# Optimization experiments

Measured on AMD Instinct MI355X. Metric: run time of the kernel, lower is better.

The kernel has to match this reference:

```python
import jax, jax.numpy as jnp
import numpy as np
from functools import partial

DELTA_B = 30.0
DELTA_H = 30.0
NB = 12  # 360/30
NH = 12
E, H, A, MLP, T = 16, 32, 32, 128, 20


def setup_inputs() -> dict:
    key = jax.random.key(0)
    ks = jax.random.split(key, 32)
    B, N = 512, 32
    inp = {}
    inp['x'] = jax.random.normal(ks[0], (B, N, T, 2), jnp.float32)
    inp['dmat'] = jax.random.uniform(ks[1], (B, N, T, N), jnp.float32) * 10.0
    inp['bmat'] = jax.random.uniform(ks[2], (B, N, T, N), jnp.float32) * 360.0
    inp['hmat'] = jax.random.uniform(ks[3], (B, N, T, N), jnp.float32) * 360.0
    inp['mask'] = jnp.ones((B, N, T), jnp.float32)
    g = lambda k, sh, s=0.1: jax.random.normal(k, sh, jnp.float32) * s
    inp['emb_w'] = g(ks[4], (2, E)); inp['emb_b'] = jnp.zeros((E,), jnp.float32)
    inp['w_ih'] = g(ks[5], (E, 4 * H)); inp['w_hh'] = g(ks[6], (H, 4 * H))
    inp['b_ih'] = jnp.zeros((4 * H,), jnp.float32); inp['b_hh'] = jnp.zeros((4 * H,), jnp.float32)
    inp['enc2att_w'] = g(ks[7], (H, A)); inp['enc2att_b'] = jnp.zeros((A,), jnp.float32)
    inp['domain_tab'] = jnp.full((NB, NH), 5.0, jnp.float32)  # domain_parameter init
    inp['spemb_w'] = g(ks[8], (2 * A, A)); inp['spemb_b'] = jnp.zeros((A,), jnp.float32)
    inp['att2enc_w'] = g(ks[9], (A, H)); inp['att2enc_b'] = jnp.zeros((H,), jnp.float32)
    inp['cls_w1'] = g(ks[10], (T * H, MLP)); inp['cls_b1'] = jnp.zeros((MLP,), jnp.float32)
    inp['cls_w2'] = g(ks[11], (MLP, MLP)); inp['cls_b2'] = jnp.zeros((MLP,), jnp.float32)
    inp['cls_w3'] = g(ks[12], (MLP, 1)); inp['cls_b3'] = jnp.zeros((1,), jnp.float32)
    return inp


def _forward(x, dmat, bmat, hmat, mask, emb_w, emb_b, w_ih, w_hh, b_ih, b_hh,
             enc2att_w, enc2att_b, domain_tab, spemb_w, spemb_b,
             att2enc_w, att2enc_b, cls_w1, cls_b1, cls_w2, cls_b2, cls_w3, cls_b3):
    B, N = x.shape[0], x.shape[1]
    xe = x @ emb_w + emb_b                      # [B,N,T,E]
    # time-major sequences for scan
    seq = (jnp.moveaxis(xe, 2, 0), jnp.moveaxis(dmat, 2, 0), jnp.moveaxis(bmat, 2, 0),
           jnp.moveaxis(hmat, 2, 0), jnp.moveaxis(mask, 2, 0))
    h0 = jnp.zeros((B, N, H), xe.dtype)
    c0 = jnp.zeros((B, N, H), xe.dtype)

    def step(carry, inp):
        h, c = carry
        x_t, d_t, b_t, hd_t, m_t = inp
        gates = x_t @ w_ih + h @ w_hh + (b_ih + b_hh)   # [B,N,4H]
        i, f, g, o = jnp.split(gates, 4, axis=-1)
        c_new = jax.nn.sigmoid(f) * c + jax.nn.sigmoid(i) * jnp.tanh(g)
        h_lstm = jax.nn.sigmoid(o) * jnp.tanh(c_new)
        ha = h_lstm @ enc2att_w + enc2att_b              # enc2att -> [B,N,A]
        # spatial attention: domain value from bearing/heading bins vs distance
        ib = jnp.clip(jnp.floor(b_t / DELTA_B), 0, NB - 1).astype(jnp.int32)
        ih = jnp.clip(jnp.floor(hd_t / DELTA_H), 0, NH - 1).astype(jnp.int32)
        w = jax.nn.relu(domain_tab[ib, ih] - d_t)        # [B,N,N]
        w = w * m_t[:, :, None] * m_t[:, None, :]
        w = w / (w.sum(-1, keepdims=True) + 1e-8)
        att = jnp.einsum('bij,bjd->bid', w, ha)          # neighbor-weighted hidden
        emb = jnp.tanh(jnp.concatenate([ha, att], -1) @ spemb_w + spemb_b)
        h_new = emb @ att2enc_w + att2enc_b              # back to hidden_size
        return (h_new, c_new), h_new

    (_, _), hs = jax.lax.scan(step, (h0, c0), seq)       # hs: [T,B,N,H]
    enc = jnp.moveaxis(hs, 0, 2).reshape(B, N, T * H)
    z = jax.nn.leaky_relu(enc @ cls_w1 + cls_b1, 0.2)
    z = jax.nn.leaky_relu(z @ cls_w2 + cls_b2, 0.2)
    return jax.nn.sigmoid(z @ cls_w3 + cls_b3)           # [B,N,1]


def reference(x, dmat, bmat, hmat, mask, emb_w, emb_b, w_ih, w_hh, b_ih, b_hh,
              enc2att_w, enc2att_b, domain_tab, spemb_w, spemb_b,
              att2enc_w, att2enc_b, cls_w1, cls_b1, cls_w2, cls_b2, cls_w3, cls_b3):
    return _forward(x, dmat, bmat, hmat, mask, emb_w, emb_b, w_ih, w_hh, b_ih, b_hh,
                    enc2att_w, enc2att_b, domain_tab, spemb_w, spemb_b,
                    att2enc_w, att2enc_b, cls_w1, cls_b1, cls_w2, cls_b2, cls_w3, cls_b3)
```

## Files before the change

kernel.cpp:

```cpp
#include <hip/hip_runtime.h>
#include <hip/hip_bf16.h>

#define TD_B 512

typedef __bf16 bf16x8 __attribute__((ext_vector_type(8)));
typedef __bf16 bf16x4 __attribute__((ext_vector_type(4)));
typedef float  f32x4  __attribute__((ext_vector_type(4)));

#define MFMA(a, b, c) __builtin_amdgcn_mfma_f32_16x16x32_bf16((a), (b), (c), 0, 0, 0)

__device__ __forceinline__ float sigf(float x)  { return 1.0f / (1.0f + __expf(-x)); }
__device__ __forceinline__ float tanhf_(float x){ return 2.0f / (1.0f + __expf(-2.0f * x)) - 1.0f; }

extern "C" __global__ void __launch_bounds__(256, 2)
traj_disc_kernel(const float* __restrict__ x, const float* __restrict__ dmat,
                 const float* __restrict__ bmat, const float* __restrict__ hmat,
                 const float* __restrict__ mask,
                 const float* __restrict__ emb_w, const float* __restrict__ emb_b,
                 const float* __restrict__ w_ih, const float* __restrict__ w_hh,
                 const float* __restrict__ b_ih, const float* __restrict__ b_hh,
                 const float* __restrict__ e2a_w, const float* __restrict__ e2a_b,
                 const float* __restrict__ dom,
                 const float* __restrict__ sp_w, const float* __restrict__ sp_b,
                 const float* __restrict__ a2e_w, const float* __restrict__ a2e_b,
                 const float* __restrict__ w1, const float* __restrict__ b1,
                 const float* __restrict__ w2, const float* __restrict__ b2,
                 const float* __restrict__ w3, const float* __restrict__ b3,
                 float* __restrict__ out)
{
    const int b    = blockIdx.x;
    const int tid  = threadIdx.x;
    const int lane = tid & 63;
    const int w    = tid >> 6;
    const int l15  = lane & 15;
    const int lg   = lane >> 4;

    __shared__ __bf16 sAin[32][72];
    __shared__ __bf16 sHl [32][40];
    __shared__ __bf16 sWN [32][40];
    __shared__ __bf16 sHaT[32][40];
    __shared__ __bf16 sEmb[32][40];
    __shared__ __bf16 sPA [32][72];
    __shared__ float  sMaskT[20][36];
    __shared__ float  sDom[144];
    __shared__ __bf16 z1bf[32][136];
    __shared__ __bf16 z2bf[32][136];

    for (int idx = tid; idx < 32 * 72; idx += 256)
        (&sAin[0][0])[idx] = (idx % 72 == 48) ? (__bf16)1.0f : (__bf16)0.0f;
    for (int idx = tid; idx < 640; idx += 256) {
        int tt = idx >> 5, n = idx & 31;
        sMaskT[tt][n] = mask[(b * 32 + n) * 20 + tt];
    }
    if (tid < 144) sDom[tid] = dom[tid];

    const int i0 = tid >> 3, p0 = tid & 7;
    const float ewa0 = emb_w[2 * p0],      ewa1 = emb_w[2 * p0 + 1];
    const float ewb0 = emb_w[16 + 2 * p0], ewb1 = emb_w[16 + 2 * p0 + 1];
    const float eb0  = emb_b[2 * p0],      eb1  = emb_b[2 * p0 + 1];

    bf16x8 Ag[2][2];
    #pragma unroll
    for (int mtl = 0; mtl < 2; ++mtl) {
        int c  = (2 * w + mtl) * 16 + l15;
        int cg = (c & 3) * 32 + (c >> 2);
        #pragma unroll
        for (int kt = 0; kt < 2; ++kt)
            #pragma unroll
            for (int j = 0; j < 8; ++j) {
                int k = kt * 32 + lg * 8 + j;
                float v;
                if (k < 16)       v = w_ih[k * 128 + cg];
                else if (k < 48)  v = w_hh[(k - 16) * 128 + cg];
                else if (k == 48) v = b_ih[cg] + b_hh[cg];
                else              v = 0.0f;
                Ag[mtl][kt][j] = (__bf16)v;
            }
    }
    const int mtw = w >> 1, ntw = w & 1;
    const int cw  = ntw * 16 + l15;
    bf16x8 Be2a, Ba2e, Bsp[2];
    #pragma unroll
    for (int j = 0; j < 8; ++j) {
        Be2a[j] = (__bf16)e2a_w[(lg * 8 + j) * 32 + cw];
        Ba2e[j] = (__bf16)a2e_w[(lg * 8 + j) * 32 + cw];
    }
    #pragma unroll
    for (int kt = 0; kt < 2; ++kt)
        #pragma unroll
        for (int j = 0; j < 8; ++j)
            Bsp[kt][j] = (__bf16)sp_w[(kt * 32 + lg * 8 + j) * 32 + cw];
    const float bEw = e2a_b[cw], bSw = sp_b[cw], bAw = a2e_b[cw];

    float cst[2][2] = {{0.f, 0.f}, {0.f, 0.f}};
    f32x4 accZ[2][2] = {};
    bf16x8 Bw1cur[2];

    float4 pdv, pbv, phv; float px0, px1;
    {
        int base = ((b * 32 + i0) * 20 + 0) * 32 + 4 * p0;
        pdv = *(const float4*)(dmat + base);
        pbv = *(const float4*)(bmat + base);
        phv = *(const float4*)(hmat + base);
        int xb = ((b * 32 + i0) * 20 + 0) * 2;
        px0 = x[xb]; px1 = x[xb + 1];
    }
    __syncthreads();

    #pragma unroll 1
    for (int t = 0; t < 20; ++t) {
        {
            float4 dv = pdv, bv = pbv, hv = phv;
            float xx0 = px0, xx1 = px1;
            if (t < 19) {
                int base = ((b * 32 + i0) * 20 + (t + 1)) * 32 + 4 * p0;
                pdv = *(const float4*)(dmat + base);
                pbv = *(const float4*)(bmat + base);
                phv = *(const float4*)(hmat + base);
                int xb = ((b * 32 + i0) * 20 + (t + 1)) * 2;
                px0 = x[xb]; px1 = x[xb + 1];
            }
            float4 mj = *(const float4*)&sMaskT[t][4 * p0];
            float  mi = sMaskT[t][i0];
            float wq[4];
            #pragma unroll
            for (int q = 0; q < 4; ++q) {
                float bq = (&bv.x)[q], hq = (&hv.x)[q];
                int ib = (int)floorf(bq * (1.0f / 30.0f)); ib = ib < 0 ? 0 : (ib > 11 ? 11 : ib);
                int ih = (int)floorf(hq * (1.0f / 30.0f)); ih = ih < 0 ? 0 : (ih > 11 ? 11 : ih);
                float v = sDom[ib * 12 + ih] - (&dv.x)[q];
                v = v > 0.f ? v : 0.f;
                wq[q] = v * (&mj.x)[q];
            }
            float s = wq[0] + wq[1] + wq[2] + wq[3];
            s += __shfl_xor(s, 1); s += __shfl_xor(s, 2); s += __shfl_xor(s, 4);
            float inv = mi / (mi * s + 1e-8f);
            bf16x4 wn4;
            #pragma unroll
            for (int q = 0; q < 4; ++q) wn4[q] = (__bf16)(wq[q] * inv);
            *(bf16x4*)&sWN[i0][4 * p0] = wn4;
            sAin[i0][2 * p0]     = (__bf16)(xx0 * ewa0 + xx1 * ewb0 + eb0);
            sAin[i0][2 * p0 + 1] = (__bf16)(xx0 * ewa1 + xx1 * ewb1 + eb1);
        }
        __syncthreads();

        {
            bf16x8 bxh[2][2];
            #pragma unroll
            for (int nt = 0; nt < 2; ++nt)
                #pragma unroll
                for (int kt = 0; kt < 2; ++kt)
                    bxh[nt][kt] = *(const bf16x8*)&sAin[nt * 16 + l15][kt * 32 + lg * 8];
            if (t >= 1) {
                bf16x8 az[2];
                #pragma unroll
                for (int mt = 0; mt < 2; ++mt)
                    az[mt] = *(const bf16x8*)&sAin[mt * 16 + l15][16 + lg * 8];
                #pragma unroll
                for (int mt = 0; mt < 2; ++mt)
                    #pragma unroll
                    for (int ntp = 0; ntp < 2; ++ntp)
                        accZ[mt][ntp] = MFMA(az[mt], Bw1cur[ntp], accZ[mt][ntp]);
            }
            #pragma unroll
            for (int mtl = 0; mtl < 2; ++mtl)
                #pragma unroll
                for (int nt = 0; nt < 2; ++nt) {
                    f32x4 cc = {0.f, 0.f, 0.f, 0.f};
                    cc = MFMA(Ag[mtl][0], bxh[nt][0], cc);
                    cc = MFMA(Ag[mtl][1], bxh[nt][1], cc);
                    float cn = sigf(cc[1]) * cst[mtl][nt] + sigf(cc[0]) * tanhf_(cc[2]);
                    cst[mtl][nt] = cn;
                    sHl[nt * 16 + l15][4 * (2 * w + mtl) + lg] = (__bf16)(sigf(cc[3]) * tanhf_(cn));
                }
            #pragma unroll
            for (int ntp = 0; ntp < 2; ++ntp) {
                int c = (2 * w + ntp) * 16 + l15;
                #pragma unroll
                for (int j = 0; j < 8; ++j)
                    Bw1cur[ntp][j] = (__bf16)w1[(t * 32 + lg * 8 + j) * 128 + c];
            }
        }
        __syncthreads();

        {
            bf16x8 a = *(const bf16x8*)&sHl[mtw * 16 + l15][lg * 8];
            f32x4 cc = {0.f, 0.f, 0.f, 0.f};
            cc = MFMA(a, Be2a, cc);
            bf16x4 tv;
            #pragma unroll
            for (int q = 0; q < 4; ++q) {
                float v = cc[q] + bEw;
                tv[q] = (__bf16)v;
                sPA[mtw * 16 + 4 * lg + q][cw] = (__bf16)v;
            }
            *(bf16x4*)&sHaT[cw][mtw * 16 + 4 * lg] = tv;
        }
        __syncthreads();

        {
            bf16x8 aW = *(const bf16x8*)&sWN [mtw * 16 + l15][lg * 8];
            bf16x8 bT = *(const bf16x8*)&sHaT[cw][lg * 8];
            f32x4 cc = {0.f, 0.f, 0.f, 0.f};
            cc = MFMA(aW, bT, cc);
            #pragma unroll
            for (int q = 0; q < 4; ++q)
                sPA[mtw * 16 + 4 * lg + q][32 + cw] = (__bf16)cc[q];
        }
        __syncthreads();

        {
            bf16x8 a0 = *(const bf16x8*)&sPA[mtw * 16 + l15][lg * 8];
            bf16x8 a1 = *(const bf16x8*)&sPA[mtw * 16 + l15][32 + lg * 8];
            f32x4 cc = {0.f, 0.f, 0.f, 0.f};
            cc = MFMA(a0, Bsp[0], cc);
            cc = MFMA(a1, Bsp[1], cc);
            #pragma unroll
            for (int q = 0; q < 4; ++q)
                sEmb[mtw * 16 + 4 * lg + q][cw] = (__bf16)tanhf_(cc[q] + bSw);
        }
        __syncthreads();

        {
            bf16x8 a = *(const bf16x8*)&sEmb[mtw * 16 + l15][lg * 8];
            f32x4 cc = {0.f, 0.f, 0.f, 0.f};
            cc = MFMA(a, Ba2e, cc);
            #pragma unroll
            for (int q = 0; q < 4; ++q)
                sAin[mtw * 16 + 4 * lg + q][16 + cw] = (__bf16)(cc[q] + bAw);
        }
        __syncthreads();
    }

    {
        bf16x8 az[2];
        #pragma unroll
        for (int mt = 0; mt < 2; ++mt)
            az[mt] = *(const bf16x8*)&sAin[mt * 16 + l15][16 + lg * 8];
        #pragma unroll
        for (int mt = 0; mt < 2; ++mt)
            #pragma unroll
            for (int ntp = 0; ntp < 2; ++ntp)
                accZ[mt][ntp] = MFMA(az[mt], Bw1cur[ntp], accZ[mt][ntp]);
    }
    #pragma unroll
    for (int mt = 0; mt < 2; ++mt)
        #pragma unroll
        for (int ntp = 0; ntp < 2; ++ntp) {
            int c = (2 * w + ntp) * 16 + l15;
            float bias = b1[c];
            #pragma unroll
            for (int q = 0; q < 4; ++q) {
                float v = accZ[mt][ntp][q] + bias;
                v = v > 0.f ? v : 0.2f * v;
                z1bf[mt * 16 + 4 * lg + q][c] = (__bf16)v;
            }
        }
    __syncthreads();

    {
        f32x4 c2[2][2] = {};
        #pragma unroll
        for (int kt = 0; kt < 4; ++kt) {
            bf16x8 a[2];
            #pragma unroll
            for (int mt = 0; mt < 2; ++mt)
                a[mt] = *(const bf16x8*)&z1bf[mt * 16 + l15][kt * 32 + lg * 8];
            bf16x8 bb[2];
            #pragma unroll
            for (int ntp = 0; ntp < 2; ++ntp) {
                int c = (2 * w + ntp) * 16 + l15;
                #pragma unroll
                for (int j = 0; j < 8; ++j)
                    bb[ntp][j] = (__bf16)w2[(kt * 32 + lg * 8 + j) * 128 + c];
            }
            #pragma unroll
            for (int mt = 0; mt < 2; ++mt)
                #pragma unroll
                for (int ntp = 0; ntp < 2; ++ntp)
                    c2[mt][ntp] = MFMA(a[mt], bb[ntp], c2[mt][ntp]);
        }
        #pragma unroll
        for (int mt = 0; mt < 2; ++mt)
            #pragma unroll
            for (int ntp = 0; ntp < 2; ++ntp) {
                int c = (2 * w + ntp) * 16 + l15;
                float bias = b2[c];
                #pragma unroll
                for (int q = 0; q < 4; ++q) {
                    float v = c2[mt][ntp][q] + bias;
                    v = v > 0.f ? v : 0.2f * v;
                    z2bf[mt * 16 + 4 * lg + q][c] = (__bf16)v;
                }
            }
    }
    __syncthreads();

    {
        int n = tid >> 3, kg = tid & 7;
        bf16x8 v0 = *(const bf16x8*)&z2bf[n][kg * 16];
        bf16x8 v1 = *(const bf16x8*)&z2bf[n][kg * 16 + 8];
        float s = 0.f;
        #pragma unroll
        for (int j = 0; j < 8; ++j)
            s += (float)v0[j] * w3[kg * 16 + j] + (float)v1[j] * w3[kg * 16 + 8 + j];
        s += __shfl_xor(s, 1); s += __shfl_xor(s, 2); s += __shfl_xor(s, 4);
        if (kg == 0) out[b * 32 + n] = sigf(s + b3[0]);
    }
}

extern "C" void kernel_launch(void* const* d_in, const int* in_sizes, int n_in,
                              void* d_out, int out_size, void* d_ws, size_t ws_size,
                              hipStream_t stream) {
    (void)in_sizes; (void)n_in; (void)d_ws; (void)ws_size; (void)out_size;
    const float* x     = (const float*)d_in[0];
    const float* dmat  = (const float*)d_in[1];
    const float* bmat  = (const float*)d_in[2];
    const float* hmat  = (const float*)d_in[3];
    const float* mask  = (const float*)d_in[4];
    const float* emb_w = (const float*)d_in[5];
    const float* emb_b = (const float*)d_in[6];
    const float* w_ih  = (const float*)d_in[7];
    const float* w_hh  = (const float*)d_in[8];
    const float* b_ih  = (const float*)d_in[9];
    const float* b_hh  = (const float*)d_in[10];
    const float* e2a_w = (const float*)d_in[11];
    const float* e2a_b = (const float*)d_in[12];
    const float* dom   = (const float*)d_in[13];
    const float* sp_w  = (const float*)d_in[14];
    const float* sp_b  = (const float*)d_in[15];
    const float* a2e_w = (const float*)d_in[16];
    const float* a2e_b = (const float*)d_in[17];
    const float* w1    = (const float*)d_in[18];
    const float* b1    = (const float*)d_in[19];
    const float* w2    = (const float*)d_in[20];
    const float* b2    = (const float*)d_in[21];
    const float* w3    = (const float*)d_in[22];
    const float* b3    = (const float*)d_in[23];
    float* out = (float*)d_out;

    traj_disc_kernel<<<dim3(TD_B), dim3(256), 0, stream>>>(
        x, dmat, bmat, hmat, mask, emb_w, emb_b, w_ih, w_hh, b_ih, b_hh,
        e2a_w, e2a_b, dom, sp_w, sp_b, a2e_w, a2e_b,
        w1, b1, w2, b2, w3, b3, out);
}
```

Measured before the change: 72.71 us.

## Process two batch items per 512-thread block and merge attention stages

Each block now handles two batch elements with 8 waves instead of one with 4, so the LSTM gate weights (Ag) are held once per wave and applied to 64 rows. The per-step pipeline merges the e2a, attention and spemb/a2e stages so they share fewer barriers, dropping from six to three __syncthreads per timestep. The w1 prefetch is moved to the start of the step so its latency overlaps more work. The grid halves to 256 blocks, which on a many-CU GPU may leave CUs idle and raises per-block LDS and register pressure.

```diff
diff --git a/kernel.cpp b/kernel.cpp
--- a/kernel.cpp
+++ b/kernel.cpp
@@ -1,7 +1,5 @@
 #include <hip/hip_runtime.h>
 #include <hip/hip_bf16.h>
-
-#define TD_B 512
 
 typedef __bf16 bf16x8 __attribute__((ext_vector_type(8)));
 typedef __bf16 bf16x4 __attribute__((ext_vector_type(4)));
@@ -12,7 +10,7 @@
 __device__ __forceinline__ float sigf(float x)  { return 1.0f / (1.0f + __expf(-x)); }
 __device__ __forceinline__ float tanhf_(float x){ return 2.0f / (1.0f + __expf(-2.0f * x)) - 1.0f; }
 
-extern "C" __global__ void __launch_bounds__(256, 2)
+extern "C" __global__ void __launch_bounds__(512, 2)
 traj_disc_kernel(const float* __restrict__ x, const float* __restrict__ dmat,
                  const float* __restrict__ bmat, const float* __restrict__ hmat,
                  const float* __restrict__ mask,
@@ -28,41 +26,42 @@
                  const float* __restrict__ w3, const float* __restrict__ b3,
                  float* __restrict__ out)
 {
-    const int b    = blockIdx.x;
+    const int b0   = blockIdx.x * 2;
     const int tid  = threadIdx.x;
     const int lane = tid & 63;
     const int w    = tid >> 6;
     const int l15  = lane & 15;
     const int lg   = lane >> 4;
 
-    __shared__ __bf16 sAin[32][72];
-    __shared__ __bf16 sHl [32][40];
-    __shared__ __bf16 sWN [32][40];
-    __shared__ __bf16 sHaT[32][40];
-    __shared__ __bf16 sEmb[32][40];
-    __shared__ __bf16 sPA [32][72];
-    __shared__ float  sMaskT[20][36];
+    __shared__ __bf16 sAin[64][72];
+    __shared__ __bf16 sHl [64][40];
+    __shared__ __bf16 sWN [64][40];
+    __shared__ __bf16 sHaT[64][40];
+    __shared__ __bf16 sEmb[64][40];
+    __shared__ __bf16 sPA [64][72];
+    __shared__ float  sMaskT[20][2][36];
     __shared__ float  sDom[144];
-    __shared__ __bf16 z1bf[32][136];
-    __shared__ __bf16 z2bf[32][136];
-
-    for (int idx = tid; idx < 32 * 72; idx += 256)
+    __shared__ __bf16 z1bf[64][136];
+    __shared__ __bf16 z2bf[64][136];
+
+    for (int idx = tid; idx < 64 * 72; idx += 512)
         (&sAin[0][0])[idx] = (idx % 72 == 48) ? (__bf16)1.0f : (__bf16)0.0f;
-    for (int idx = tid; idx < 640; idx += 256) {
-        int tt = idx >> 5, n = idx & 31;
-        sMaskT[tt][n] = mask[(b * 32 + n) * 20 + tt];
+    for (int idx = tid; idx < 1280; idx += 512) {
+        int tt = idx >> 6, r = idx & 63;
+        sMaskT[tt][r >> 5][r & 31] = mask[((b0 + (r >> 5)) * 32 + (r & 31)) * 20 + tt];
     }
     if (tid < 144) sDom[tid] = dom[tid];
 
     const int i0 = tid >> 3, p0 = tid & 7;
+    const int wbA = i0 >> 5, iA = i0 & 31;
+    const int bbA = b0 + wbA;
     const float ewa0 = emb_w[2 * p0],      ewa1 = emb_w[2 * p0 + 1];
     const float ewb0 = emb_w[16 + 2 * p0], ewb1 = emb_w[16 + 2 * p0 + 1];
     const float eb0  = emb_b[2 * p0],      eb1  = emb_b[2 * p0 + 1];
 
-    bf16x8 Ag[2][2];
-    #pragma unroll
-    for (int mtl = 0; mtl < 2; ++mtl) {
-        int c  = (2 * w + mtl) * 16 + l15;
+    bf16x8 Ag[2];
+    {
+        int c  = 16 * w + l15;
         int cg = (c & 3) * 32 + (c >> 2);
         #pragma unroll
         for (int kt = 0; kt < 2; ++kt)
@@ -74,12 +73,12 @@
                 else if (k < 48)  v = w_hh[(k - 16) * 128 + cg];
                 else if (k == 48) v = b_ih[cg] + b_hh[cg];
                 else              v = 0.0f;
-                Ag[mtl][kt][j] = (__bf16)v;
-            }
-    }
-    const int mtw = w >> 1, ntw = w & 1;
-    const int cw  = ntw * 16 + l15;
-    bf16x8 Be2a, Ba2e, Bsp[2];
+                Ag[kt][j] = (__bf16)v;
+            }
+    }
+    const int wb = w >> 2, mtw = (w >> 1) & 1, ntw = w & 1;
+    const int cw = ntw * 16 + l15;
+    bf16x8 Be2a, Ba2e, Bsp[2][2];
     #pragma unroll
     for (int j = 0; j < 8; ++j) {
         Be2a[j] = (__bf16)e2a_w[(lg * 8 + j) * 32 + cw];
@@ -88,21 +87,25 @@
     #pragma unroll
     for (int kt = 0; kt < 2; ++kt)
         #pragma unroll
-        for (int j = 0; j < 8; ++j)
-            Bsp[kt][j] = (__bf16)sp_w[(kt * 32 + lg * 8 + j) * 32 + cw];
-    const float bEw = e2a_b[cw], bSw = sp_b[cw], bAw = a2e_b[cw];
-
-    float cst[2][2] = {{0.f, 0.f}, {0.f, 0.f}};
-    f32x4 accZ[2][2] = {};
-    bf16x8 Bw1cur[2];
+        for (int nt2 = 0; nt2 < 2; ++nt2)
+            #pragma unroll
+            for (int j = 0; j < 8; ++j)
+                Bsp[kt][nt2][j] = (__bf16)sp_w[(kt * 32 + lg * 8 + j) * 32 + nt2 * 16 + l15];
+    const float bEw = e2a_b[cw], bAw = a2e_b[cw];
+    const float bS2[2] = { sp_b[l15], sp_b[16 + l15] };
+
+    float cst[4] = {0.f, 0.f, 0.f, 0.f};
+    f32x4 accZ[4] = {};
+    bf16x8 Bw1cur, Bw1nxt;
+    const int c1 = 16 * w + l15;
 
     float4 pdv, pbv, phv; float px0, px1;
     {
-        int base = ((b * 32 + i0) * 20 + 0) * 32 + 4 * p0;
+        int base = ((bbA * 32 + iA) * 20 + 0) * 32 + 4 * p0;
         pdv = *(const float4*)(dmat + base);
         pbv = *(const float4*)(bmat + base);
         phv = *(const float4*)(hmat + base);
-        int xb = ((b * 32 + i0) * 20 + 0) * 2;
+        int xb = ((bbA * 32 + iA) * 20 + 0) * 2;
         px0 = x[xb]; px1 = x[xb + 1];
     }
     __syncthreads();
@@ -110,18 +113,21 @@
     #pragma unroll 1
     for (int t = 0; t < 20; ++t) {
         {
+            #pragma unroll
+            for (int j = 0; j < 8; ++j)
+                Bw1nxt[j] = (__bf16)w1[(t * 32 + lg * 8 + j) * 128 + c1];
             float4 dv = pdv, bv = pbv, hv = phv;
             float xx0 = px0, xx1 = px1;
             if (t < 19) {
-                int base = ((b * 32 + i0) * 20 + (t + 1)) * 32 + 4 * p0;
+                int base = ((bbA * 32 + iA) * 20 + (t + 1)) * 32 + 4 * p0;
                 pdv = *(const float4*)(dmat + base);
                 pbv = *(const float4*)(bmat + base);
                 phv = *(const float4*)(hmat + base);
-                int xb = ((b * 32 + i0) * 20 + (t + 1)) * 2;
+                int xb = ((bbA * 32 + iA) * 20 + (t + 1)) * 2;
                 px0 = x[xb]; px1 = x[xb + 1];
             }
-            float4 mj = *(const float4*)&sMaskT[t][4 * p0];
-            float  mi = sMaskT[t][i0];
+            float4 mj = *(const float4*)&sMaskT[t][wbA][4 * p0];
+            float  mi = sMaskT[t][wbA][iA];
             float wq[4];
             #pragma unroll
             for (int q = 0; q < 4; ++q) {
@@ -145,167 +151,132 @@
         __syncthreads();
 
         {
-            bf16x8 bxh[2][2];
-            #pragma unroll
-            for (int nt = 0; nt < 2; ++nt)
+            bf16x8 az[4], bxh[4][2];
+            #pragma unroll
+            for (int rt = 0; rt < 4; ++rt) {
+                az[rt]     = *(const bf16x8*)&sAin[rt * 16 + l15][16 + lg * 8];
+                bxh[rt][0] = *(const bf16x8*)&sAin[rt * 16 + l15][lg * 8];
+                bxh[rt][1] = *(const bf16x8*)&sAin[rt * 16 + l15][32 + lg * 8];
+            }
+            if (t >= 1) {
                 #pragma unroll
-                for (int kt = 0; kt < 2; ++kt)
-                    bxh[nt][kt] = *(const bf16x8*)&sAin[nt * 16 + l15][kt * 32 + lg * 8];
-            if (t >= 1) {
-                bf16x8 az[2];
+                for (int rt = 0; rt < 4; ++rt)
+                    accZ[rt] = MFMA(az[rt], Bw1cur, accZ[rt]);
+            }
+            Bw1cur = Bw1nxt;
+            #pragma unroll
+            for (int rt = 0; rt < 4; ++rt) {
+                f32x4 cc = {0.f, 0.f, 0.f, 0.f};
+                cc = MFMA(Ag[0], bxh[rt][0], cc);
+                cc = MFMA(Ag[1], bxh[rt][1], cc);
+                float cn = sigf(cc[1]) * cst[rt] + sigf(cc[0]) * tanhf_(cc[2]);
+                cst[rt] = cn;
+                sHl[rt * 16 + l15][4 * w + lg] = (__bf16)(sigf(cc[3]) * tanhf_(cn));
+            }
+        }
+        __syncthreads();
+
+        {
+            #pragma unroll
+            for (int mt = 0; mt < 2; ++mt) {
+                bf16x8 a = *(const bf16x8*)&sHl[wb * 32 + mt * 16 + l15][lg * 8];
+                f32x4 cc = {0.f, 0.f, 0.f, 0.f};
+                cc = MFMA(a, Be2a, cc);
+                bf16x4 tv;
                 #pragma unroll
-                for (int mt = 0; mt < 2; ++mt)
-                    az[mt] = *(const bf16x8*)&sAin[mt * 16 + l15][16 + lg * 8];
-                #pragma unroll
-                for (int mt = 0; mt < 2; ++mt)
-                    #pragma unroll
-                    for (int ntp = 0; ntp < 2; ++ntp)
-                        accZ[mt][ntp] = MFMA(az[mt], Bw1cur[ntp], accZ[mt][ntp]);
-            }
-            #pragma unroll
-            for (int mtl = 0; mtl < 2; ++mtl)
-                #pragma unroll
-                for (int nt = 0; nt < 2; ++nt) {
-                    f32x4 cc = {0.f, 0.f, 0.f, 0.f};
-                    cc = MFMA(Ag[mtl][0], bxh[nt][0], cc);
-                    cc = MFMA(Ag[mtl][1], bxh[nt][1], cc);
-                    float cn = sigf(cc[1]) * cst[mtl][nt] + sigf(cc[0]) * tanhf_(cc[2]);
-                    cst[mtl][nt] = cn;
-                    sHl[nt * 16 + l15][4 * (2 * w + mtl) + lg] = (__bf16)(sigf(cc[3]) * tanhf_(cn));
+                for (int q = 0; q < 4; ++q) {
+                    float v = cc[q] + bEw;
+                    tv[q] = (__bf16)v;
+                    sPA[wb * 32 + mt * 16 + 4 * lg + q][cw] = (__bf16)v;
                 }
-            #pragma unroll
-            for (int ntp = 0; ntp < 2; ++ntp) {
-                int c = (2 * w + ntp) * 16 + l15;
-                #pragma unroll
-                for (int j = 0; j < 8; ++j)
-                    Bw1cur[ntp][j] = (__bf16)w1[(t * 32 + lg * 8 + j) * 128 + c];
-            }
-        }
-        __syncthreads();
-
-        {
-            bf16x8 a = *(const bf16x8*)&sHl[mtw * 16 + l15][lg * 8];
-            f32x4 cc = {0.f, 0.f, 0.f, 0.f};
-            cc = MFMA(a, Be2a, cc);
-            bf16x4 tv;
-            #pragma unroll
-            for (int q = 0; q < 4; ++q) {
-                float v = cc[q] + bEw;
-                tv[q] = (__bf16)v;
-                sPA[mtw * 16 + 4 * lg + q][cw] = (__bf16)v;
-            }
-            *(bf16x4*)&sHaT[cw][mtw * 16 + 4 * lg] = tv;
-        }
-        __syncthreads();
-
-        {
-            bf16x8 aW = *(const bf16x8*)&sWN [mtw * 16 + l15][lg * 8];
-            bf16x8 bT = *(const bf16x8*)&sHaT[cw][lg * 8];
+                *(bf16x4*)&sHaT[wb * 32 + cw][mt * 16 + 4 * lg] = tv;
+            }
+            bf16x8 aW = *(const bf16x8*)&sWN [wb * 32 + mtw * 16 + l15][lg * 8];
+            bf16x8 bT = *(const bf16x8*)&sHaT[wb * 32 + ntw * 16 + l15][lg * 8];
             f32x4 cc = {0.f, 0.f, 0.f, 0.f};
             cc = MFMA(aW, bT, cc);
             #pragma unroll
             for (int q = 0; q < 4; ++q)
-                sPA[mtw * 16 + 4 * lg + q][32 + cw] = (__bf16)cc[q];
+                sPA[wb * 32 + mtw * 16 + 4 * lg + q][32 + cw] = (__bf16)cc[q];
         }
         __syncthreads();
 
         {
-            bf16x8 a0 = *(const bf16x8*)&sPA[mtw * 16 + l15][lg * 8];
-            bf16x8 a1 = *(const bf16x8*)&sPA[mtw * 16 + l15][32 + lg * 8];
-            f32x4 cc = {0.f, 0.f, 0.f, 0.f};
-            cc = MFMA(a0, Bsp[0], cc);
-            cc = MFMA(a1, Bsp[1], cc);
+            bf16x8 a0 = *(const bf16x8*)&sPA[wb * 32 + mtw * 16 + l15][lg * 8];
+            bf16x8 a1 = *(const bf16x8*)&sPA[wb * 32 + mtw * 16 + l15][32 + lg * 8];
+            #pragma unroll
+            for (int nt2 = 0; nt2 < 2; ++nt2) {
+                f32x4 cc = {0.f, 0.f, 0.f, 0.f};
+                cc = MFMA(a0, Bsp[0][nt2], cc);
+                cc = MFMA(a1, Bsp[1][nt2], cc);
+                #pragma unroll
+                for (int q = 0; q < 4; ++q)
+                    sEmb[wb * 32 + mtw * 16 + 4 * lg + q][nt2 * 16 + l15] = (__bf16)tanhf_(cc[q] + bS2[nt2]);
+            }
+            bf16x8 ae = *(const bf16x8*)&sEmb[wb * 32 + mtw * 16 + l15][lg * 8];
+            f32x4 cf = {0.f, 0.f, 0.f, 0.f};
+            cf = MFMA(ae, Ba2e, cf);
             #pragma unroll
             for (int q = 0; q < 4; ++q)
-                sEmb[mtw * 16 + 4 * lg + q][cw] = (__bf16)tanhf_(cc[q] + bSw);
-        }
-        __syncthreads();
-
-        {
-            bf16x8 a = *(const bf16x8*)&sEmb[mtw * 16 + l15][lg * 8];
-            f32x4 cc = {0.f, 0.f, 0.f, 0.f};
-            cc = MFMA(a, Ba2e, cc);
-            #pragma unroll
-            for (int q = 0; q < 4; ++q)
-                sAin[mtw * 16 + 4 * lg + q][16 + cw] = (__bf16)(cc[q] + bAw);
-        }
-        __syncthreads();
-    }
-
-    {
-        bf16x8 az[2];
-        #pragma unroll
-        for (int mt = 0; mt < 2; ++mt)
-            az[mt] = *(const bf16x8*)&sAin[mt * 16 + l15][16 + lg * 8];
-        #pragma unroll
-        for (int mt = 0; mt < 2; ++mt)
-            #pragma unroll
-            for (int ntp = 0; ntp < 2; ++ntp)
-                accZ[mt][ntp] = MFMA(az[mt], Bw1cur[ntp], accZ[mt][ntp]);
-    }
-    #pragma unroll
-    for (int mt = 0; mt < 2; ++mt)
-        #pragma unroll
-        for (int ntp = 0; ntp < 2; ++ntp) {
-            int c = (2 * w + ntp) * 16 + l15;
-            float bias = b1[c];
+                sAin[wb * 32 + mtw * 16 + 4 * lg + q][16 + cw] = (__bf16)(cf[q] + bAw);
+        }
+    }
+
+    __syncthreads();
+    {
+        #pragma unroll
+        for (int rt = 0; rt < 4; ++rt) {
+            bf16x8 az = *(const bf16x8*)&sAin[rt * 16 + l15][16 + lg * 8];
+            accZ[rt] = MFMA(az, Bw1cur, accZ[rt]);
+        }
+    }
+    {
+        float bias = b1[c1];
+        #pragma unroll
+        for (int rt = 0; rt < 4; ++rt)
             #pragma unroll
             for (int q = 0; q < 4; ++q) {
-                float v = accZ[mt][ntp][q] + bias;
+                float v = accZ[rt][q] + bias;
                 v = v > 0.f ? v : 0.2f * v;
-                z1bf[mt * 16 + 4 * lg + q][c] = (__bf16)v;
-            }
-        }
+                z1bf[rt * 16 + 4 * lg + q][c1] = (__bf16)v;
+            }
+    }
     __syncthreads();
-
-    {
-        f32x4 c2[2][2] = {};
+    {
+        f32x4 c2z[4] = {};
         #pragma unroll
         for (int kt = 0; kt < 4; ++kt) {
-            bf16x8 a[2];
-            #pragma unroll
-            for (int mt = 0; mt < 2; ++mt)
-                a[mt] = *(const bf16x8*)&z1bf[mt * 16 + l15][kt * 32 + lg * 8];
-            bf16x8 bb[2];
-            #pragma unroll
-            for (int ntp = 0; ntp < 2; ++ntp) {
-                int c = (2 * w + ntp) * 16 + l15;
-                #pragma unroll
-                for (int j = 0; j < 8; ++j)
-                    bb[ntp][j] = (__bf16)w2[(kt * 32 + lg * 8 + j) * 128 + c];
-            }
-            #pragma unroll
-            for (int mt = 0; mt < 2; ++mt)
-                #pragma unroll
-                for (int ntp = 0; ntp < 2; ++ntp)
-                    c2[mt][ntp] = MFMA(a[mt], bb[ntp], c2[mt][ntp]);
-        }
-        #pragma unroll
-        for (int mt = 0; mt < 2; ++mt)
-            #pragma unroll
-            for (int ntp = 0; ntp < 2; ++ntp) {
-                int c = (2 * w + ntp) * 16 + l15;
-                float bias = b2[c];
-                #pragma unroll
-                for (int q = 0; q < 4; ++q) {
-                    float v = c2[mt][ntp][q] + bias;
-                    v = v > 0.f ? v : 0.2f * v;
-                    z2bf[mt * 16 + 4 * lg + q][c] = (__bf16)v;
-                }
+            bf16x8 bw2;
+            #pragma unroll
+            for (int j = 0; j < 8; ++j)
+                bw2[j] = (__bf16)w2[(kt * 32 + lg * 8 + j) * 128 + c1];
+            #pragma unroll
+            for (int rt = 0; rt < 4; ++rt) {
+                bf16x8 a = *(const bf16x8*)&z1bf[rt * 16 + l15][kt * 32 + lg * 8];
+                c2z[rt] = MFMA(a, bw2, c2z[rt]);
+            }
+        }
+        float bias = b2[c1];
+        #pragma unroll
+        for (int rt = 0; rt < 4; ++rt)
+            #pragma unroll
+            for (int q = 0; q < 4; ++q) {
+                float v = c2z[rt][q] + bias;
+                v = v > 0.f ? v : 0.2f * v;
+                z2bf[rt * 16 + 4 * lg + q][c1] = (__bf16)v;
             }
     }
     __syncthreads();
-
-    {
-        int n = tid >> 3, kg = tid & 7;
-        bf16x8 v0 = *(const bf16x8*)&z2bf[n][kg * 16];
-        bf16x8 v1 = *(const bf16x8*)&z2bf[n][kg * 16 + 8];
+    {
+        int n2 = tid >> 3, kg = tid & 7;
+        bf16x8 v0 = *(const bf16x8*)&z2bf[n2][kg * 16];
+        bf16x8 v1 = *(const bf16x8*)&z2bf[n2][kg * 16 + 8];
         float s = 0.f;
         #pragma unroll
         for (int j = 0; j < 8; ++j)
             s += (float)v0[j] * w3[kg * 16 + j] + (float)v1[j] * w3[kg * 16 + 8 + j];
         s += __shfl_xor(s, 1); s += __shfl_xor(s, 2); s += __shfl_xor(s, 4);
-        if (kg == 0) out[b * 32 + n] = sigf(s + b3[0]);
+        if (kg == 0) out[(b0 + (n2 >> 5)) * 32 + (n2 & 31)] = sigf(s + b3[0]);
     }
 }
 
@@ -339,7 +310,7 @@
     const float* b3    = (const float*)d_in[23];
     float* out = (float*)d_out;
 
-    traj_disc_kernel<<<dim3(TD_B), dim3(256), 0, stream>>>(
+    traj_disc_kernel<<<dim3(256), dim3(512), 0, stream>>>(
         x, dmat, bmat, hmat, mask, emb_w, emb_b, w_ih, w_hh, b_ih, b_hh,
         e2a_w, e2a_b, dom, sp_w, sp_b, a2e_w, a2e_b,
         w1, b1, w2, b2, w3, b3, out);
```

Result: slower. 80.37 us (+10.5%).

## Trade redundant per-wave MFMA work for fewer block barriers in recurrent step

Applied to the files above, without the earlier changes.

Each wave now computes the enc2att projection for both row tiles, and the spatial-embedding projection for both column tiles. It can then consume its own LDS writes without waiting on other waves, which drops three of the per-timestep __syncthreads. The cost is duplicated MFMA, tanh work and redundant, identical LDS stores across waves. The trailing barrier at the end of each time step is also removed, so correctness depends on a barrier at the start of the next iteration.

```diff
diff --git a/kernel.cpp b/kernel.cpp
--- a/kernel.cpp
+++ b/kernel.cpp
@@ -79,7 +79,7 @@
     }
     const int mtw = w >> 1, ntw = w & 1;
     const int cw  = ntw * 16 + l15;
-    bf16x8 Be2a, Ba2e, Bsp[2];
+    bf16x8 Be2a, Ba2e, Bsp[2][2];
     #pragma unroll
     for (int j = 0; j < 8; ++j) {
         Be2a[j] = (__bf16)e2a_w[(lg * 8 + j) * 32 + cw];
@@ -88,9 +88,12 @@
     #pragma unroll
     for (int kt = 0; kt < 2; ++kt)
         #pragma unroll
-        for (int j = 0; j < 8; ++j)
-            Bsp[kt][j] = (__bf16)sp_w[(kt * 32 + lg * 8 + j) * 32 + cw];
-    const float bEw = e2a_b[cw], bSw = sp_b[cw], bAw = a2e_b[cw];
+        for (int nt2 = 0; nt2 < 2; ++nt2)
+            #pragma unroll
+            for (int j = 0; j < 8; ++j)
+                Bsp[kt][nt2][j] = (__bf16)sp_w[(kt * 32 + lg * 8 + j) * 32 + nt2 * 16 + l15];
+    const float bEw = e2a_b[cw], bAw = a2e_b[cw];
+    const float bS2[2] = { sp_b[l15], sp_b[16 + l15] };
 
     float cst[2][2] = {{0.f, 0.f}, {0.f, 0.f}};
     f32x4 accZ[2][2] = {};
@@ -184,23 +187,22 @@
         __syncthreads();
 
         {
-            bf16x8 a = *(const bf16x8*)&sHl[mtw * 16 + l15][lg * 8];
-            f32x4 cc = {0.f, 0.f, 0.f, 0.f};
-            cc = MFMA(a, Be2a, cc);
-            bf16x4 tv;
-            #pragma unroll
-            for (int q = 0; q < 4; ++q) {
-                float v = cc[q] + bEw;
-                tv[q] = (__bf16)v;
-                sPA[mtw * 16 + 4 * lg + q][cw] = (__bf16)v;
-            }
-            *(bf16x4*)&sHaT[cw][mtw * 16 + 4 * lg] = tv;
-        }
-        __syncthreads();
-
-        {
+            #pragma unroll
+            for (int mt = 0; mt < 2; ++mt) {
+                bf16x8 a = *(const bf16x8*)&sHl[mt * 16 + l15][lg * 8];
+                f32x4 cc = {0.f, 0.f, 0.f, 0.f};
+                cc = MFMA(a, Be2a, cc);
+                bf16x4 tv;
+                #pragma unroll
+                for (int q = 0; q < 4; ++q) {
+                    float v = cc[q] + bEw;
+                    tv[q] = (__bf16)v;
+                    sPA[mt * 16 + 4 * lg + q][cw] = (__bf16)v;
+                }
+                *(bf16x4*)&sHaT[cw][mt * 16 + 4 * lg] = tv;
+            }
             bf16x8 aW = *(const bf16x8*)&sWN [mtw * 16 + l15][lg * 8];
-            bf16x8 bT = *(const bf16x8*)&sHaT[cw][lg * 8];
+            bf16x8 bT = *(const bf16x8*)&sHaT[ntw * 16 + l15][lg * 8];
             f32x4 cc = {0.f, 0.f, 0.f, 0.f};
             cc = MFMA(aW, bT, cc);
             #pragma unroll
@@ -212,26 +214,25 @@
         {
             bf16x8 a0 = *(const bf16x8*)&sPA[mtw * 16 + l15][lg * 8];
             bf16x8 a1 = *(const bf16x8*)&sPA[mtw * 16 + l15][32 + lg * 8];
-            f32x4 cc = {0.f, 0.f, 0.f, 0.f};
-            cc = MFMA(a0, Bsp[0], cc);
-            cc = MFMA(a1, Bsp[1], cc);
+            #pragma unroll
+            for (int nt2 = 0; nt2 < 2; ++nt2) {
+                f32x4 cc = {0.f, 0.f, 0.f, 0.f};
+                cc = MFMA(a0, Bsp[0][nt2], cc);
+                cc = MFMA(a1, Bsp[1][nt2], cc);
+                #pragma unroll
+                for (int q = 0; q < 4; ++q)
+                    sEmb[mtw * 16 + 4 * lg + q][nt2 * 16 + l15] = (__bf16)tanhf_(cc[q] + bS2[nt2]);
+            }
+            bf16x8 ae = *(const bf16x8*)&sEmb[mtw * 16 + l15][lg * 8];
+            f32x4 cf = {0.f, 0.f, 0.f, 0.f};
+            cf = MFMA(ae, Ba2e, cf);
             #pragma unroll
             for (int q = 0; q < 4; ++q)
-                sEmb[mtw * 16 + 4 * lg + q][cw] = (__bf16)tanhf_(cc[q] + bSw);
-        }
-        __syncthreads();
-
-        {
-            bf16x8 a = *(const bf16x8*)&sEmb[mtw * 16 + l15][lg * 8];
-            f32x4 cc = {0.f, 0.f, 0.f, 0.f};
-            cc = MFMA(a, Ba2e, cc);
-            #pragma unroll
-            for (int q = 0; q < 4; ++q)
-                sAin[mtw * 16 + 4 * lg + q][16 + cw] = (__bf16)(cc[q] + bAw);
-        }
-        __syncthreads();
-    }
-
+                sAin[mtw * 16 + 4 * lg + q][16 + cw] = (__bf16)(cf[q] + bAw);
+        }
+    }
+
+    __syncthreads();
     {
         bf16x8 az[2];
         #pragma unroll
```

Result: slower. 77.90 us (+7.1%).

## Process two batch items per block to amortize barriers and interleave MFMA chains

Applied to the files above, without the earlier changes.

Each block now handles two batch elements with duplicated shared buffers and per-item state, and the grid shrinks to 256 blocks. The serial per-timestep chain of barriers and small dependent MFMAs is shared across two independent items, which gives more instruction-level parallelism per barrier and halves the barrier count per item. The trailing barrier of each timestep is also dropped, since the next step's first phase does not touch the buffers written last. The cost is more registers and LDS per block (launch bounds lowered to 1 block per SM) and only 256 blocks, which may underfill the GPU's 256 CUs or reduce latency hiding.

```diff
diff --git a/kernel.cpp b/kernel.cpp
--- a/kernel.cpp
+++ b/kernel.cpp
@@ -1,7 +1,5 @@
 #include <hip/hip_runtime.h>
 #include <hip/hip_bf16.h>
-
-#define TD_B 512
 
 typedef __bf16 bf16x8 __attribute__((ext_vector_type(8)));
 typedef __bf16 bf16x4 __attribute__((ext_vector_type(4)));
@@ -12,7 +10,7 @@
 __device__ __forceinline__ float sigf(float x)  { return 1.0f / (1.0f + __expf(-x)); }
 __device__ __forceinline__ float tanhf_(float x){ return 2.0f / (1.0f + __expf(-2.0f * x)) - 1.0f; }
 
-extern "C" __global__ void __launch_bounds__(256, 2)
+extern "C" __global__ void __launch_bounds__(256, 1)
 traj_disc_kernel(const float* __restrict__ x, const float* __restrict__ dmat,
                  const float* __restrict__ bmat, const float* __restrict__ hmat,
                  const float* __restrict__ mask,
@@ -28,29 +26,30 @@
                  const float* __restrict__ w3, const float* __restrict__ b3,
                  float* __restrict__ out)
 {
-    const int b    = blockIdx.x;
+    const int b0   = blockIdx.x * 2;
     const int tid  = threadIdx.x;
     const int lane = tid & 63;
     const int w    = tid >> 6;
     const int l15  = lane & 15;
     const int lg   = lane >> 4;
 
-    __shared__ __bf16 sAin[32][72];
-    __shared__ __bf16 sHl [32][40];
-    __shared__ __bf16 sWN [32][40];
-    __shared__ __bf16 sHaT[32][40];
-    __shared__ __bf16 sEmb[32][40];
-    __shared__ __bf16 sPA [32][72];
-    __shared__ float  sMaskT[20][36];
+    __shared__ __bf16 sAin[2][32][72];
+    __shared__ __bf16 sHl [2][32][40];
+    __shared__ __bf16 sWN [2][32][40];
+    __shared__ __bf16 sHaT[2][32][40];
+    __shared__ __bf16 sEmb[2][32][40];
+    __shared__ __bf16 sPA [2][32][72];
+    __shared__ float  sMaskT[2][20][36];
     __shared__ float  sDom[144];
-    __shared__ __bf16 z1bf[32][136];
-    __shared__ __bf16 z2bf[32][136];
-
-    for (int idx = tid; idx < 32 * 72; idx += 256)
-        (&sAin[0][0])[idx] = (idx % 72 == 48) ? (__bf16)1.0f : (__bf16)0.0f;
-    for (int idx = tid; idx < 640; idx += 256) {
-        int tt = idx >> 5, n = idx & 31;
-        sMaskT[tt][n] = mask[(b * 32 + n) * 20 + tt];
+    __shared__ __bf16 z1bf[2][32][136];
+    __shared__ __bf16 z2bf[2][32][136];
+
+    for (int idx = tid; idx < 2 * 32 * 72; idx += 256)
+        (&sAin[0][0][0])[idx] = (idx % 72 == 48) ? (__bf16)1.0f : (__bf16)0.0f;
+    for (int idx = tid; idx < 1280; idx += 256) {
+        int u = idx / 640, r = idx % 640;
+        int tt = r >> 5, n = r & 31;
+        sMaskT[u][tt][n] = mask[((b0 + u) * 32 + n) * 20 + tt];
     }
     if (tid < 144) sDom[tid] = dom[tid];
 
@@ -92,36 +91,38 @@
             Bsp[kt][j] = (__bf16)sp_w[(kt * 32 + lg * 8 + j) * 32 + cw];
     const float bEw = e2a_b[cw], bSw = sp_b[cw], bAw = a2e_b[cw];
 
-    float cst[2][2] = {{0.f, 0.f}, {0.f, 0.f}};
-    f32x4 accZ[2][2] = {};
+    float cst[2][2][2] = {};
+    f32x4 accZ[2][2][2] = {};
     bf16x8 Bw1cur[2];
 
-    float4 pdv, pbv, phv; float px0, px1;
-    {
-        int base = ((b * 32 + i0) * 20 + 0) * 32 + 4 * p0;
-        pdv = *(const float4*)(dmat + base);
-        pbv = *(const float4*)(bmat + base);
-        phv = *(const float4*)(hmat + base);
-        int xb = ((b * 32 + i0) * 20 + 0) * 2;
-        px0 = x[xb]; px1 = x[xb + 1];
+    float4 pdv[2], pbv[2], phv[2]; float px0[2], px1[2];
+    #pragma unroll
+    for (int u = 0; u < 2; ++u) {
+        int base = (((b0 + u) * 32 + i0) * 20 + 0) * 32 + 4 * p0;
+        pdv[u] = *(const float4*)(dmat + base);
+        pbv[u] = *(const float4*)(bmat + base);
+        phv[u] = *(const float4*)(hmat + base);
+        int xb = (((b0 + u) * 32 + i0) * 20 + 0) * 2;
+        px0[u] = x[xb]; px1[u] = x[xb + 1];
     }
     __syncthreads();
 
     #pragma unroll 1
     for (int t = 0; t < 20; ++t) {
-        {
-            float4 dv = pdv, bv = pbv, hv = phv;
-            float xx0 = px0, xx1 = px1;
+        #pragma unroll
+        for (int u = 0; u < 2; ++u) {
+            float4 dv = pdv[u], bv = pbv[u], hv = phv[u];
+            float xx0 = px0[u], xx1 = px1[u];
             if (t < 19) {
-                int base = ((b * 32 + i0) * 20 + (t + 1)) * 32 + 4 * p0;
-                pdv = *(const float4*)(dmat + base);
-                pbv = *(const float4*)(bmat + base);
-                phv = *(const float4*)(hmat + base);
-                int xb = ((b * 32 + i0) * 20 + (t + 1)) * 2;
-                px0 = x[xb]; px1 = x[xb + 1];
-            }
-            float4 mj = *(const float4*)&sMaskT[t][4 * p0];
-            float  mi = sMaskT[t][i0];
+                int base = (((b0 + u) * 32 + i0) * 20 + (t + 1)) * 32 + 4 * p0;
+                pdv[u] = *(const float4*)(dmat + base);
+                pbv[u] = *(const float4*)(bmat + base);
+                phv[u] = *(const float4*)(hmat + base);
+                int xb = (((b0 + u) * 32 + i0) * 20 + (t + 1)) * 2;
+                px0[u] = x[xb]; px1[u] = x[xb + 1];
+            }
+            float4 mj = *(const float4*)&sMaskT[u][t][4 * p0];
+            float  mi = sMaskT[u][t][i0];
             float wq[4];
             #pragma unroll
             for (int q = 0; q < 4; ++q) {
@@ -138,29 +139,28 @@
             bf16x4 wn4;
             #pragma unroll
             for (int q = 0; q < 4; ++q) wn4[q] = (__bf16)(wq[q] * inv);
-            *(bf16x4*)&sWN[i0][4 * p0] = wn4;
-            sAin[i0][2 * p0]     = (__bf16)(xx0 * ewa0 + xx1 * ewb0 + eb0);
-            sAin[i0][2 * p0 + 1] = (__bf16)(xx0 * ewa1 + xx1 * ewb1 + eb1);
-        }
-        __syncthreads();
-
-        {
+            *(bf16x4*)&sWN[u][i0][4 * p0] = wn4;
+            sAin[u][i0][2 * p0]     = (__bf16)(xx0 * ewa0 + xx1 * ewb0 + eb0);
+            sAin[u][i0][2 * p0 + 1] = (__bf16)(xx0 * ewa1 + xx1 * ewb1 + eb1);
+        }
+        __syncthreads();
+
+        #pragma unroll
+        for (int u = 0; u < 2; ++u) {
             bf16x8 bxh[2][2];
             #pragma unroll
             for (int nt = 0; nt < 2; ++nt)
                 #pragma unroll
                 for (int kt = 0; kt < 2; ++kt)
-                    bxh[nt][kt] = *(const bf16x8*)&sAin[nt * 16 + l15][kt * 32 + lg * 8];
+                    bxh[nt][kt] = *(const bf16x8*)&sAin[u][nt * 16 + l15][kt * 32 + lg * 8];
             if (t >= 1) {
-                bf16x8 az[2];
-                #pragma unroll
-                for (int mt = 0; mt < 2; ++mt)
-                    az[mt] = *(const bf16x8*)&sAin[mt * 16 + l15][16 + lg * 8];
-                #pragma unroll
-                for (int mt = 0; mt < 2; ++mt)
+                #pragma unroll
+                for (int mt = 0; mt < 2; ++mt) {
+                    bf16x8 az = *(const bf16x8*)&sAin[u][mt * 16 + l15][16 + lg * 8];
                     #pragma unroll
                     for (int ntp = 0; ntp < 2; ++ntp)
-                        accZ[mt][ntp] = MFMA(az[mt], Bw1cur[ntp], accZ[mt][ntp]);
+                        accZ[u][mt][ntp] = MFMA(az, Bw1cur[ntp], accZ[u][mt][ntp]);
+                }
             }
             #pragma unroll
             for (int mtl = 0; mtl < 2; ++mtl)
@@ -169,22 +169,23 @@
                     f32x4 cc = {0.f, 0.f, 0.f, 0.f};
                     cc = MFMA(Ag[mtl][0], bxh[nt][0], cc);
                     cc = MFMA(Ag[mtl][1], bxh[nt][1], cc);
-                    float cn = sigf(cc[1]) * cst[mtl][nt] + sigf(cc[0]) * tanhf_(cc[2]);
-                    cst[mtl][nt] = cn;
-                    sHl[nt * 16 + l15][4 * (2 * w + mtl) + lg] = (__bf16)(sigf(cc[3]) * tanhf_(cn));
+                    float cn = sigf(cc[1]) * cst[u][mtl][nt] + sigf(cc[0]) * tanhf_(cc[2]);
+                    cst[u][mtl][nt] = cn;
+                    sHl[u][nt * 16 + l15][4 * (2 * w + mtl) + lg] = (__bf16)(sigf(cc[3]) * tanhf_(cn));
                 }
-            #pragma unroll
-            for (int ntp = 0; ntp < 2; ++ntp) {
-                int c = (2 * w + ntp) * 16 + l15;
-                #pragma unroll
-                for (int j = 0; j < 8; ++j)
-                    Bw1cur[ntp][j] = (__bf16)w1[(t * 32 + lg * 8 + j) * 128 + c];
-            }
-        }
-        __syncthreads();
-
-        {
-            bf16x8 a = *(const bf16x8*)&sHl[mtw * 16 + l15][lg * 8];
+        }
+        #pragma unroll
+        for (int ntp = 0; ntp < 2; ++ntp) {
+            int c = (2 * w + ntp) * 16 + l15;
+            #pragma unroll
+            for (int j = 0; j < 8; ++j)
+                Bw1cur[ntp][j] = (__bf16)w1[(t * 32 + lg * 8 + j) * 128 + c];
+        }
+        __syncthreads();
+
+        #pragma unroll
+        for (int u = 0; u < 2; ++u) {
+            bf16x8 a = *(const bf16x8*)&sHl[u][mtw * 16 + l15][lg * 8];
             f32x4 cc = {0.f, 0.f, 0.f, 0.f};
             cc = MFMA(a, Be2a, cc);
             bf16x4 tv;
@@ -192,80 +193,83 @@
             for (int q = 0; q < 4; ++q) {
                 float v = cc[q] + bEw;
                 tv[q] = (__bf16)v;
-                sPA[mtw * 16 + 4 * lg + q][cw] = (__bf16)v;
-            }
-            *(bf16x4*)&sHaT[cw][mtw * 16 + 4 * lg] = tv;
-        }
-        __syncthreads();
-
-        {
-            bf16x8 aW = *(const bf16x8*)&sWN [mtw * 16 + l15][lg * 8];
-            bf16x8 bT = *(const bf16x8*)&sHaT[cw][lg * 8];
+                sPA[u][mtw * 16 + 4 * lg + q][cw] = (__bf16)v;
+            }
+            *(bf16x4*)&sHaT[u][cw][mtw * 16 + 4 * lg] = tv;
+        }
+        __syncthreads();
+
+        #pragma unroll
+        for (int u = 0; u < 2; ++u) {
+            bf16x8 aW = *(const bf16x8*)&sWN [u][mtw * 16 + l15][lg * 8];
+            bf16x8 bT = *(const bf16x8*)&sHaT[u][cw][lg * 8];
             f32x4 cc = {0.f, 0.f, 0.f, 0.f};
             cc = MFMA(aW, bT, cc);
             #pragma unroll
             for (int q = 0; q < 4; ++q)
-                sPA[mtw * 16 + 4 * lg + q][32 + cw] = (__bf16)cc[q];
-        }
-        __syncthreads();
-
-        {
-            bf16x8 a0 = *(const bf16x8*)&sPA[mtw * 16 + l15][lg * 8];
-            bf16x8 a1 = *(const bf16x8*)&sPA[mtw * 16 + l15][32 + lg * 8];
+                sPA[u][mtw * 16 + 4 * lg + q][32 + cw] = (__bf16)cc[q];
+        }
+        __syncthreads();
+
+        #pragma unroll
+        for (int u = 0; u < 2; ++u) {
+            bf16x8 a0 = *(const bf16x8*)&sPA[u][mtw * 16 + l15][lg * 8];
+            bf16x8 a1 = *(const bf16x8*)&sPA[u][mtw * 16 + l15][32 + lg * 8];
             f32x4 cc = {0.f, 0.f, 0.f, 0.f};
             cc = MFMA(a0, Bsp[0], cc);
             cc = MFMA(a1, Bsp[1], cc);
             #pragma unroll
             for (int q = 0; q < 4; ++q)
-                sEmb[mtw * 16 + 4 * lg + q][cw] = (__bf16)tanhf_(cc[q] + bSw);
-        }
-        __syncthreads();
-
-        {
-            bf16x8 a = *(const bf16x8*)&sEmb[mtw * 16 + l15][lg * 8];
-            f32x4 cc = {0.f, 0.f, 0.f, 0.f};
-            cc = MFMA(a, Ba2e, cc);
+                sEmb[u][mtw * 16 + 4 * lg + q][cw] = (__bf16)tanhf_(cc[q] + bSw);
+        }
+        __syncthreads();
+
+        #pragma unroll
+        for (int u = 0; u < 2; ++u) {
+            bf16x8 ae = *(const bf16x8*)&sEmb[u][mtw * 16 + l15][lg * 8];
+            f32x4 cf = {0.f, 0.f, 0.f, 0.f};
+            cf = MFMA(ae, Ba2e, cf);
             #pragma unroll
             for (int q = 0; q < 4; ++q)
-                sAin[mtw * 16 + 4 * lg + q][16 + cw] = (__bf16)(cc[q] + bAw);
-        }
-        __syncthreads();
-    }
-
-    {
-        bf16x8 az[2];
+                sAin[u][mtw * 16 + 4 * lg + q][16 + cw] = (__bf16)(cf[q] + bAw);
+        }
+    }
+
+    __syncthreads();
+    #pragma unroll
+    for (int u = 0; u < 2; ++u) {
+        #pragma unroll
+        for (int mt = 0; mt < 2; ++mt) {
+            bf16x8 az = *(const bf16x8*)&sAin[u][mt * 16 + l15][16 + lg * 8];
+            #pragma unroll
+            for (int ntp = 0; ntp < 2; ++ntp)
+                accZ[u][mt][ntp] = MFMA(az, Bw1cur[ntp], accZ[u][mt][ntp]);
+        }
         #pragma unroll
         for (int mt = 0; mt < 2; ++mt)
-            az[mt] = *(const bf16x8*)&sAin[mt * 16 + l15][16 + lg * 8];
-        #pragma unroll
-        for (int mt = 0; mt < 2; ++mt)
-            #pragma unroll
-            for (int ntp = 0; ntp < 2; ++ntp)
-                accZ[mt][ntp] = MFMA(az[mt], Bw1cur[ntp], accZ[mt][ntp]);
-    }
-    #pragma unroll
-    for (int mt = 0; mt < 2; ++mt)
-        #pragma unroll
-        for (int ntp = 0; ntp < 2; ++ntp) {
-            int c = (2 * w + ntp) * 16 + l15;
-            float bias = b1[c];
-            #pragma unroll
-            for (int q = 0; q < 4; ++q) {
-                float v = accZ[mt][ntp][q] + bias;
-                v = v > 0.f ? v : 0.2f * v;
-                z1bf[mt * 16 + 4 * lg + q][c] = (__bf16)v;
-            }
-        }
+            #pragma unroll
+            for (int ntp = 0; ntp < 2; ++ntp) {
+                int c = (2 * w + ntp) * 16 + l15;
+                float bias = b1[c];
+                #pragma unroll
+                for (int q = 0; q < 4; ++q) {
+                    float v = accZ[u][mt][ntp][q] + bias;
+                    v = v > 0.f ? v : 0.2f * v;
+                    z1bf[u][mt * 16 + 4 * lg + q][c] = (__bf16)v;
+                }
+            }
+    }
     __syncthreads();
 
-    {
+    #pragma unroll
+    for (int u = 0; u < 2; ++u) {
         f32x4 c2[2][2] = {};
         #pragma unroll
         for (int kt = 0; kt < 4; ++kt) {
             bf16x8 a[2];
             #pragma unroll
             for (int mt = 0; mt < 2; ++mt)
-                a[mt] = *(const bf16x8*)&z1bf[mt * 16 + l15][kt * 32 + lg * 8];
+                a[mt] = *(const bf16x8*)&z1bf[u][mt * 16 + l15][kt * 32 + lg * 8];
             bf16x8 bb[2];
             #pragma unroll
             for (int ntp = 0; ntp < 2; ++ntp) {
@@ -290,22 +294,23 @@
                 for (int q = 0; q < 4; ++q) {
                     float v = c2[mt][ntp][q] + bias;
                     v = v > 0.f ? v : 0.2f * v;
-                    z2bf[mt * 16 + 4 * lg + q][c] = (__bf16)v;
+                    z2bf[u][mt * 16 + 4 * lg + q][c] = (__bf16)v;
                 }
             }
     }
     __syncthreads();
 
-    {
+    #pragma unroll
+    for (int u = 0; u < 2; ++u) {
         int n = tid >> 3, kg = tid & 7;
-        bf16x8 v0 = *(const bf16x8*)&z2bf[n][kg * 16];
-        bf16x8 v1 = *(const bf16x8*)&z2bf[n][kg * 16 + 8];
+        bf16x8 v0 = *(const bf16x8*)&z2bf[u][n][kg * 16];
+        bf16x8 v1 = *(const bf16x8*)&z2bf[u][n][kg * 16 + 8];
         float s = 0.f;
         #pragma unroll
         for (int j = 0; j < 8; ++j)
             s += (float)v0[j] * w3[kg * 16 + j] + (float)v1[j] * w3[kg * 16 + 8 + j];
         s += __shfl_xor(s, 1); s += __shfl_xor(s, 2); s += __shfl_xor(s, 4);
-        if (kg == 0) out[b * 32 + n] = sigf(s + b3[0]);
+        if (kg == 0) out[(b0 + u) * 32 + n] = sigf(s + b3[0]);
     }
 }
 
@@ -339,7 +344,7 @@
     const float* b3    = (const float*)d_in[23];
     float* out = (float*)d_out;
 
-    traj_disc_kernel<<<dim3(TD_B), dim3(256), 0, stream>>>(
+    traj_disc_kernel<<<dim3(256), dim3(256), 0, stream>>>(
         x, dmat, bmat, hmat, mask, emb_w, emb_b, w_ih, w_hh, b_ih, b_hh,
         e2a_w, e2a_b, dom, sp_w, sp_b, a2e_w, a2e_b,
         w1, b1, w2, b2, w3, b3, out);
```

Measured after the change: 101.6 us. 1.4x slower.
